# Optimization experiments

Measured on AMD Instinct MI355X. Metric: run time of the kernel, lower is better.

Reference implementation:

```python
import jax, jax.numpy as jnp
import numpy as np

EMBED_DIM = 1024
HEADS = 16


def setup_inputs() -> dict:
    key = jax.random.key(0)
    ks = jax.random.split(key, 9)
    d = EMBED_DIM
    s = 1.0 / np.sqrt(d)
    x = jax.random.normal(ks[0], (4, 2048, d), dtype=jnp.float32)
    return {
        "x": x,
        "Wq": jax.random.uniform(ks[1], (d, d), jnp.float32, -s, s),
        "bq": jax.random.uniform(ks[2], (d,), jnp.float32, -s, s),
        "Wk": jax.random.uniform(ks[3], (d, d), jnp.float32, -s, s),
        "bk": jax.random.uniform(ks[4], (d,), jnp.float32, -s, s),
        "Wv": jax.random.uniform(ks[5], (d, d), jnp.float32, -s, s),
        "bv": jax.random.uniform(ks[6], (d,), jnp.float32, -s, s),
        "Wo": jax.random.uniform(ks[7], (d, d), jnp.float32, -s, s),
        "bo": jax.random.uniform(ks[8], (d,), jnp.float32, -s, s),
    }


def reference(x, Wq, bq, Wk, bk, Wv, bv, Wo, bo):
    B, N, C = x.shape
    H = HEADS
    Dh = C // H
    scale = Dh ** (-0.5)
    # Linear projections (torch Linear: x @ W.T + b), split heads -> [B,H,N,Dh]
    def split_heads(t):
        return t.reshape(B, N, H, Dh).transpose(0, 2, 1, 3)
    q = split_heads(x @ Wq.T + bq)
    k = split_heads(x @ Wk.T + bk)
    v = split_heads(x @ Wv.T + bv)
    attn = jnp.einsum('bhnd,bhmd->bhnm', q, k) * scale  # [B,H,N,N]
    attn = jax.nn.softmax(attn, axis=-1)
    # dropout ratio is 0.0 (eval); abs() kept for faithfulness
    out = jnp.einsum('bhnm,bhmd->bhnd', jnp.abs(attn), v)
    out = out.transpose(0, 2, 1, 3).reshape(B, N, C)
    return out @ Wo.T + bo
```

## Files before the change

kernel.cpp:

```cpp
#include <hip/hip_runtime.h>
#include <hip/hip_bf16.h>
#include <cstddef>
#include <cstdint>

namespace {
constexpr int Bn = 4, SEQ = 2048, CDIM = 1024, NH = 16, DH = 64;
constexpr int Mrows = Bn * SEQ;
}

using bf16x8 = __attribute__((ext_vector_type(8))) __bf16;
using f32x4  = __attribute__((ext_vector_type(4))) float;
using f32x16 = __attribute__((ext_vector_type(16))) float;

#define MFMA16(a, b, c) __builtin_amdgcn_mfma_f32_16x16x32_bf16(a, b, c, 0, 0, 0)
#define MFMA32(a, b, c) __builtin_amdgcn_mfma_f32_32x32x16_bf16(a, b, c, 0, 0, 0)

__device__ __forceinline__ void gload_lds16(const __bf16* g, __bf16* l) {
  __builtin_amdgcn_global_load_lds(
      (const __attribute__((address_space(1))) void*)g,
      (__attribute__((address_space(3))) void*)l, 16, 0, 0);
}

__device__ __forceinline__ unsigned pk2(float a, float b) {
  union { __bf16 h[2]; unsigned u; } x;
  x.h[0] = (__bf16)a; x.h[1] = (__bf16)b;
  return x.u;
}

__global__ __launch_bounds__(256) void cast_inputs(
    const float* __restrict__ x, const float* __restrict__ wq,
    const float* __restrict__ wk, const float* __restrict__ wv,
    const float* __restrict__ wo, __bf16* __restrict__ xb,
    __bf16* __restrict__ wall) {
  constexpr int X4 = Mrows * CDIM / 4;
  constexpr int W4 = CDIM * CDIM / 4;
  constexpr int total = X4 + 4 * W4;
  for (int i = blockIdx.x * 256 + threadIdx.x; i < total; i += gridDim.x * 256) {
    const float4* src;
    __bf16* dst;
    int o;
    if (i < X4) {
      src = (const float4*)x; dst = xb; o = i;
    } else {
      int j = i - X4;
      int w = j >> 18;
      o = j & (W4 - 1);
      src = (const float4*)(w == 0 ? wq : w == 1 ? wk : w == 2 ? wv : wo);
      dst = wall + (size_t)w * (CDIM * CDIM);
    }
    float4 v = src[o];
    union { __bf16 h[4]; ushort4 u4; } pk;
    pk.h[0] = (__bf16)v.x; pk.h[1] = (__bf16)v.y;
    pk.h[2] = (__bf16)v.z; pk.h[3] = (__bf16)v.w;
    *(ushort4*)(dst + (size_t)o * 4) = pk.u4;
  }
}

template <int MODE>
__global__ __launch_bounds__(256) void gemm_mfma(
    const __bf16* __restrict__ A, const __bf16* __restrict__ Bw,
    const float* __restrict__ b0, const float* __restrict__ b1,
    const float* __restrict__ b2, __bf16* __restrict__ Qb,
    __bf16* __restrict__ Kb, __bf16* __restrict__ Vb,
    float* __restrict__ Yf) {
  __shared__ __align__(16) __bf16 As[128 * 32];
  __shared__ __align__(16) __bf16 Bs[128 * 32];
  const int tid = threadIdx.x;
  const int lane = tid & 63, w = tid >> 6;
  const int wr = w >> 1, wc = w & 1;
  const int l4 = lane >> 4, l15 = lane & 15;
  const int m0 = blockIdx.y * 128, n0 = blockIdx.x * 128;

  f32x4 acc[4][4] = {};
  const int srow = lane >> 2;
  const int scol = (lane & 3) * 8;

  for (int k0 = 0; k0 < CDIM; k0 += 32) {
    __syncthreads();
#pragma unroll
    for (int u = 0; u < 2; ++u) {
      const int c = w * 2 + u;
      gload_lds16(A + (size_t)(m0 + c * 16 + srow) * CDIM + k0 + scol,
                  &As[c * 512]);
      gload_lds16(Bw + (size_t)(n0 + c * 16 + srow) * CDIM + k0 + scol,
                  &Bs[c * 512]);
    }
    __syncthreads();
    bf16x8 af[4], bfr[4];
#pragma unroll
    for (int i = 0; i < 4; ++i)
      af[i] = *(const bf16x8*)&As[(wr * 64 + i * 16 + l15) * 32 + l4 * 8];
#pragma unroll
    for (int j = 0; j < 4; ++j)
      bfr[j] = *(const bf16x8*)&Bs[(wc * 64 + j * 16 + l15) * 32 + l4 * 8];
#pragma unroll
    for (int i = 0; i < 4; ++i)
#pragma unroll
      for (int j = 0; j < 4; ++j)
        acc[i][j] = MFMA16(af[i], bfr[j], acc[i][j]);
  }

  const int row0 = m0 + wr * 64;
  if (MODE == 0) {
#pragma unroll
    for (int j = 0; j < 4; ++j) {
      const int n = (n0 + wc * 64 + j * 16) + l15;
      const float bias = b0[n];
#pragma unroll
      for (int i = 0; i < 4; ++i) {
        const int mrow = row0 + i * 16 + l4 * 4;
#pragma unroll
        for (int r = 0; r < 4; ++r)
          Yf[(size_t)(mrow + r) * CDIM + n] = acc[i][j][r] + bias;
      }
    }
  } else {
    const int which = n0 >> 10;
    const float* bias = which == 0 ? b0 : which == 1 ? b1 : b2;
    __bf16* Out = which == 0 ? Qb : which == 1 ? Kb : Vb;
    const float scl = which == 0 ? 0.125f : 1.0f;
    const int n0c = n0 & 1023;
#pragma unroll
    for (int j = 0; j < 4; ++j) {
      const int c = n0c + wc * 64 + j * 16 + l15;
      const int h = c >> 6, dh = c & 63;
      const float bias_v = bias[c];
#pragma unroll
      for (int i = 0; i < 4; ++i) {
        const int mrow = row0 + i * 16 + l4 * 4;
#pragma unroll
        for (int r = 0; r < 4; ++r) {
          const int m = mrow + r;
          const int b_ = m >> 11, ns = m & (SEQ - 1);
          Out[((size_t)(b_ * NH + h) * SEQ + ns) * DH + dh] =
              (__bf16)((acc[i][j][r] + bias_v) * scl);
        }
      }
    }
  }
}

__global__ __launch_bounds__(256) void attn_mfma(
    const __bf16* __restrict__ Qg, const __bf16* __restrict__ Kg,
    const __bf16* __restrict__ Vg, __bf16* __restrict__ AO) {
  __shared__ __align__(16) __bf16 vT[2][64][72];
  const int tid = threadIdx.x, lane = tid & 63, w = tid >> 6;
  const int l31 = lane & 31, hi = lane >> 5;
  const int bh = blockIdx.x, qt = blockIdx.y;
  const int b_ = bh >> 4, h_ = bh & 15;

  const __bf16* Qp = Qg + ((size_t)bh * SEQ + qt * 128 + w * 32) * DH;
  const __bf16* Kb = Kg + (size_t)bh * SEQ * DH;
  const __bf16* Vb = Vg + (size_t)bh * SEQ * DH;

  bf16x8 q[4];
#pragma unroll
  for (int t = 0; t < 4; ++t)
    q[t] = *(const bf16x8*)(Qp + (size_t)l31 * DH + t * 16 + hi * 8);

  f32x16 o0 = {}, o1 = {};
  float m_i = -1e30f, l_i = 0.f;

  const int vkey = tid & 63, vdg = (tid >> 6) * 16;

  bf16x8 kfA[8], kfB[8];
  auto kload = [&](bf16x8(&kf)[8], int kt) {
#pragma unroll
    for (int c = 0; c < 2; ++c)
#pragma unroll
      for (int t = 0; t < 4; ++t)
        kf[c * 4 + t] = *(const bf16x8*)(
            Kb + ((size_t)kt * 64 + c * 32 + l31) * DH + t * 16 + hi * 8);
  };
  kload(kfA, 0);

  auto body = [&](bf16x8(&kc)[8], bf16x8(&kn)[8], int kt, int buf) {
    const __bf16* Vt = Vb + (size_t)kt * 64 * DH;
    bf16x8 vr0 = *(const bf16x8*)(Vt + (size_t)vkey * DH + vdg);
    bf16x8 vr1 = *(const bf16x8*)(Vt + (size_t)vkey * DH + vdg + 8);
    f32x16 s0 = {}, s1 = {};
#pragma unroll
    for (int t = 0; t < 4; ++t) {
      s0 = MFMA32(kc[t], q[t], s0);
      s1 = MFMA32(kc[4 + t], q[t], s1);
    }
    kload(kn, (kt + 1) & 31);
#pragma unroll
    for (int e = 0; e < 8; ++e) vT[buf][vdg + e][vkey] = vr0[e];
#pragma unroll
    for (int e = 0; e < 8; ++e) vT[buf][vdg + 8 + e][vkey] = vr1[e];
    float mx = s0[0];
#pragma unroll
    for (int j = 1; j < 16; ++j) mx = fmaxf(mx, s0[j]);
#pragma unroll
    for (int j = 0; j < 16; ++j) mx = fmaxf(mx, s1[j]);
    mx = fmaxf(mx, __shfl_xor(mx, 32));
    if (!__all(mx <= m_i + 8.0f)) {
      const float mnew = fmaxf(m_i, mx);
      const float alpha = __expf(m_i - mnew);
      m_i = mnew;
      l_i *= alpha;
      o0 *= alpha;
      o1 *= alpha;
    }
    unsigned W0[4][2], W1[4][2];
    float ps = 0.f;
#pragma unroll
    for (int m = 0; m < 4; ++m)
#pragma unroll
      for (int j2 = 0; j2 < 2; ++j2) {
        float a0 = __expf(s0[4 * m + 2 * j2] - m_i);
        float a1 = __expf(s0[4 * m + 2 * j2 + 1] - m_i);
        float b0 = __expf(s1[4 * m + 2 * j2] - m_i);
        float b1 = __expf(s1[4 * m + 2 * j2 + 1] - m_i);
        ps += (a0 + a1) + (b0 + b1);
        W0[m][j2] = pk2(a0, a1);
        W1[m][j2] = pk2(b0, b1);
      }
    ps += __shfl_xor(ps, 32);
    l_i += ps;
    bf16x8 Bp[4];
#pragma unroll
    for (int X = 0; X < 2; ++X)
#pragma unroll
      for (int k2 = 0; k2 < 2; ++k2) {
        union { unsigned u[4]; bf16x8 v; } bb;
#pragma unroll
        for (int j2 = 0; j2 < 2; ++j2) {
          const unsigned a = X ? W1[2 * k2][j2] : W0[2 * k2][j2];
          const unsigned b = X ? W1[2 * k2 + 1][j2] : W0[2 * k2 + 1][j2];
          const unsigned snd = hi ? a : b;
          const unsigned rcv = __shfl_xor(snd, 32);
          bb.u[j2] = hi ? rcv : a;
          bb.u[2 + j2] = hi ? b : rcv;
        }
        Bp[X * 2 + k2] = bb.v;
      }
    __syncthreads();
#pragma unroll
    for (int ks = 0; ks < 4; ++ks) {
      bf16x8 va0 = *(const bf16x8*)&vT[buf][l31][ks * 16 + hi * 8];
      bf16x8 va1 = *(const bf16x8*)&vT[buf][32 + l31][ks * 16 + hi * 8];
      o0 = MFMA32(va0, Bp[ks], o0);
      o1 = MFMA32(va1, Bp[ks], o1);
    }
  };

#pragma unroll 1
  for (int kt2 = 0; kt2 < 16; ++kt2) {
    body(kfA, kfB, 2 * kt2, 0);
    body(kfB, kfA, 2 * kt2 + 1, 1);
  }

  const float inv = 1.f / l_i;
  const int qglob = qt * 128 + w * 32 + l31;
  __bf16* aorow = AO + ((size_t)(b_ * SEQ) + qglob) * CDIM + h_ * DH;
#pragma unroll
  for (int u = 0; u < 8; ++u) {
    const int dbase = 8 * (u >> 1) + 4 * hi + 2 * (u & 1);
    *(unsigned*)(aorow + dbase) = pk2(o0[2 * u] * inv, o0[2 * u + 1] * inv);
    *(unsigned*)(aorow + 32 + dbase) = pk2(o1[2 * u] * inv, o1[2 * u + 1] * inv);
  }
}

extern "C" void kernel_launch(void* const* d_in, const int* in_sizes, int n_in,
                              void* d_out, int out_size, void* d_ws,
                              size_t ws_size, hipStream_t stream) {
  const float* x  = (const float*)d_in[0];
  const float* Wq = (const float*)d_in[1];
  const float* bq = (const float*)d_in[2];
  const float* Wk = (const float*)d_in[3];
  const float* bk = (const float*)d_in[4];
  const float* Wv = (const float*)d_in[5];
  const float* bv = (const float*)d_in[6];
  const float* Wo = (const float*)d_in[7];
  const float* bo = (const float*)d_in[8];
  float* out = (float*)d_out;

  __bf16* xb   = (__bf16*)d_ws;
  __bf16* wall = xb + (size_t)Mrows * CDIM;
  __bf16* Qb   = wall + (size_t)4 * CDIM * CDIM;
  __bf16* Kb   = Qb + (size_t)Mrows * CDIM;
  __bf16* Vb   = Kb + (size_t)Mrows * CDIM;
  __bf16* AO   = Vb + (size_t)Mrows * CDIM;

  cast_inputs<<<2048, 256, 0, stream>>>(x, Wq, Wk, Wv, Wo, xb, wall);
  gemm_mfma<1><<<dim3(24, 64), 256, 0, stream>>>(xb, wall, bq, bk, bv, Qb, Kb,
                                                 Vb, nullptr);
  attn_mfma<<<dim3(Bn * NH, SEQ / 128), 256, 0, stream>>>(Qb, Kb, Vb, AO);
  gemm_mfma<0><<<dim3(8, 64), 256, 0, stream>>>(
      AO, wall + (size_t)3 * CDIM * CDIM, bo, nullptr, nullptr, nullptr,
      nullptr, nullptr, out);
}
```

Before: 344.4 us.

## Prefetch V one tile ahead, move barrier earlier, add MFMA priority hints

The attention kernel now loads the next V tile into registers one iteration early, alongside the next K tile, and issues both loads before the QK^T MFMAs. The current V is then written to LDS, and the barrier is moved right after that write, ahead of the softmax. It also wraps the MFMA blocks in s_setprio, uses tree reductions for the row max and row sum, and sets a 4-waves-per-SIMD launch bound. The goal is to hide global load latency and shorten dependency chains, at the cost of extra registers that the occupancy bound may force to spill.

```diff
diff --git a/kernel.cpp b/kernel.cpp
--- a/kernel.cpp
+++ b/kernel.cpp
@@ -140,7 +140,7 @@
   }
 }
 
-__global__ __launch_bounds__(256) void attn_mfma(
+__global__ __launch_bounds__(256, 4) void attn_mfma(
     const __bf16* __restrict__ Qg, const __bf16* __restrict__ Kg,
     const __bf16* __restrict__ Vg, __bf16* __restrict__ AO) {
   __shared__ __align__(16) __bf16 vT[2][64][72];
@@ -164,6 +164,7 @@
   const int vkey = tid & 63, vdg = (tid >> 6) * 16;
 
   bf16x8 kfA[8], kfB[8];
+  bf16x8 vfA[2], vfB[2];
   auto kload = [&](bf16x8(&kf)[8], int kt) {
 #pragma unroll
     for (int c = 0; c < 2; ++c)
@@ -172,29 +173,41 @@
         kf[c * 4 + t] = *(const bf16x8*)(
             Kb + ((size_t)kt * 64 + c * 32 + l31) * DH + t * 16 + hi * 8);
   };
+  auto vload = [&](bf16x8(&vf)[2], int kt) {
+    const __bf16* Vt = Vb + (size_t)kt * 64 * DH;
+    vf[0] = *(const bf16x8*)(Vt + (size_t)vkey * DH + vdg);
+    vf[1] = *(const bf16x8*)(Vt + (size_t)vkey * DH + vdg + 8);
+  };
   kload(kfA, 0);
-
-  auto body = [&](bf16x8(&kc)[8], bf16x8(&kn)[8], int kt, int buf) {
-    const __bf16* Vt = Vb + (size_t)kt * 64 * DH;
-    bf16x8 vr0 = *(const bf16x8*)(Vt + (size_t)vkey * DH + vdg);
-    bf16x8 vr1 = *(const bf16x8*)(Vt + (size_t)vkey * DH + vdg + 8);
+  vload(vfA, 0);
+
+  auto body = [&](bf16x8(&kc)[8], bf16x8(&kn)[8], bf16x8(&vc)[2],
+                  bf16x8(&vn)[2], int kt, int buf) {
+    const int ktn = (kt + 1) & 31;
+    vload(vn, ktn);
+    kload(kn, ktn);
     f32x16 s0 = {}, s1 = {};
+    __builtin_amdgcn_s_setprio(1);
 #pragma unroll
     for (int t = 0; t < 4; ++t) {
       s0 = MFMA32(kc[t], q[t], s0);
       s1 = MFMA32(kc[4 + t], q[t], s1);
     }
-    kload(kn, (kt + 1) & 31);
-#pragma unroll
-    for (int e = 0; e < 8; ++e) vT[buf][vdg + e][vkey] = vr0[e];
-#pragma unroll
-    for (int e = 0; e < 8; ++e) vT[buf][vdg + 8 + e][vkey] = vr1[e];
-    float mx = s0[0];
-#pragma unroll
-    for (int j = 1; j < 16; ++j) mx = fmaxf(mx, s0[j]);
-#pragma unroll
-    for (int j = 0; j < 16; ++j) mx = fmaxf(mx, s1[j]);
-    mx = fmaxf(mx, __shfl_xor(mx, 32));
+    __builtin_amdgcn_s_setprio(0);
+#pragma unroll
+    for (int e = 0; e < 8; ++e) vT[buf][vdg + e][vkey] = vc[0][e];
+#pragma unroll
+    for (int e = 0; e < 8; ++e) vT[buf][vdg + 8 + e][vkey] = vc[1][e];
+    __syncthreads();
+    float mt[16];
+#pragma unroll
+    for (int j = 0; j < 16; ++j) mt[j] = fmaxf(s0[j], s1[j]);
+#pragma unroll
+    for (int st = 8; st > 0; st >>= 1)
+#pragma unroll
+      for (int j = 0; j < 8; ++j)
+        if (j < st) mt[j] = fmaxf(mt[j], mt[j + st]);
+    float mx = fmaxf(mt[0], __shfl_xor(mt[0], 32));
     if (!__all(mx <= m_i + 8.0f)) {
       const float mnew = fmaxf(m_i, mx);
       const float alpha = __expf(m_i - mnew);
@@ -204,7 +217,7 @@
       o1 *= alpha;
     }
     unsigned W0[4][2], W1[4][2];
-    float ps = 0.f;
+    float psa[4] = {0.f, 0.f, 0.f, 0.f};
 #pragma unroll
     for (int m = 0; m < 4; ++m)
 #pragma unroll
@@ -213,10 +226,11 @@
         float a1 = __expf(s0[4 * m + 2 * j2 + 1] - m_i);
         float b0 = __expf(s1[4 * m + 2 * j2] - m_i);
         float b1 = __expf(s1[4 * m + 2 * j2 + 1] - m_i);
-        ps += (a0 + a1) + (b0 + b1);
+        psa[m] += (a0 + a1) + (b0 + b1);
         W0[m][j2] = pk2(a0, a1);
         W1[m][j2] = pk2(b0, b1);
       }
+    float ps = (psa[0] + psa[1]) + (psa[2] + psa[3]);
     ps += __shfl_xor(ps, 32);
     l_i += ps;
     bf16x8 Bp[4];
@@ -236,7 +250,7 @@
         }
         Bp[X * 2 + k2] = bb.v;
       }
-    __syncthreads();
+    __builtin_amdgcn_s_setprio(1);
 #pragma unroll
     for (int ks = 0; ks < 4; ++ks) {
       bf16x8 va0 = *(const bf16x8*)&vT[buf][l31][ks * 16 + hi * 8];
@@ -244,12 +258,13 @@
       o0 = MFMA32(va0, Bp[ks], o0);
       o1 = MFMA32(va1, Bp[ks], o1);
     }
+    __builtin_amdgcn_s_setprio(0);
   };
 
 #pragma unroll 1
   for (int kt2 = 0; kt2 < 16; ++kt2) {
-    body(kfA, kfB, 2 * kt2, 0);
-    body(kfB, kfA, 2 * kt2 + 1, 1);
+    body(kfA, kfB, vfA, vfB, 2 * kt2, 0);
+    body(kfB, kfA, vfB, vfA, 2 * kt2 + 1, 1);
   }
 
   const float inv = 1.f / l_i;
```

New measurement: 547.5 us. 1.59x slower.
